# Kernel optimization log

Measured on AMD Instinct MI355X. Metric: run time of the kernel, lower is better.

## Reference

```python
import jax, jax.numpy as jnp
import numpy as np

N_NODES = 500_000
DIM_IN = 128
DIM_OUT = 128
N_DISTRICTS = 1024


def setup_inputs() -> dict:
    key = jax.random.key(0)
    k_x, k_z, k_w1, k_w2 = jax.random.split(key, 4)
    x = jax.random.normal(k_x, (N_NODES, DIM_IN), dtype=jnp.float32)
    zone_lst = jax.random.randint(k_z, (N_NODES,), 0, N_DISTRICTS, dtype=jnp.int64)
    # MLP params: Linear(dim_in, 2*dim_in), Linear(2*dim_in, dim_out)
    w1 = jax.random.normal(k_w1, (DIM_IN, 2 * DIM_IN), dtype=jnp.float32) * (1.0 / np.sqrt(DIM_IN))
    b1 = jnp.zeros((2 * DIM_IN,), dtype=jnp.float32)
    w2 = jax.random.normal(k_w2, (2 * DIM_IN, DIM_OUT), dtype=jnp.float32) * (1.0 / np.sqrt(2 * DIM_IN))
    b2 = jnp.zeros((DIM_OUT,), dtype=jnp.float32)
    return {"x": x, "zone_lst": zone_lst, "w1": w1, "b1": b1, "w2": w2, "b2": b2}


def reference(x, zone_lst, w1, b1, w2, b2):
    # Per-district sum of node features: one fused segment reduction
    # (replaces the python loop over districts in the original).
    head = jax.ops.segment_sum(x, zone_lst, num_segments=N_DISTRICTS)  # [D, dim_in]
    # MLP: ReLU -> Linear -> ReLU -> Linear
    h = jnp.maximum(head, 0.0)
    h = jnp.maximum(h @ w1 + b1, 0.0)
    return h @ w2 + b2
```

## Files before the change

kernel.cpp:

```cpp
#include <hip/hip_runtime.h>

#define DIM_IN 128
#define DIM_HID 256
#define DIM_OUT 128
#define N_DIST 1024
#define NB 256


__device__ __forceinline__ int detect_is64(const int* __restrict__ zone_raw,
                                           int t, int* s_flag) {
    if (t < 64) {
        bool hi_zero = (zone_raw[2 * t + 1] == 0);
        unsigned long long m = __ballot(hi_zero);
        if (t == 0) *s_flag = (m == ~0ull) ? 1 : 0;
    }
    __syncthreads();
    return *s_flag;
}

__global__ __launch_bounds__(256)
void hist_kernel(const int* __restrict__ zone, int n,
                 int* __restrict__ blockHist) {
    __shared__ int lhist[N_DIST];
    __shared__ int s_is64;
    const int t = threadIdx.x;
    const int b = blockIdx.x;
    for (int i = t; i < N_DIST; i += 256) lhist[i] = 0;
    const int is64 = detect_is64(zone, t, &s_is64);

    const int chunk = (n + NB - 1) / NB;
    const int start = b * chunk;
    const int end = min(n, start + chunk);
    const long long* zone64 = (const long long*)zone;
    for (int i = start + t; i < end; i += 256) {
        int z = is64 ? (int)zone64[i] : zone[i];
        atomicAdd(&lhist[z], 1);
    }
    __syncthreads();
    for (int i = t; i < N_DIST; i += 256) blockHist[b * N_DIST + i] = lhist[i];
}

__global__ __launch_bounds__(1024)
void scan_kernel(int* __restrict__ blockHist,
                 int* __restrict__ offsets, int* __restrict__ counts) {
    __shared__ int tmp[N_DIST];
    const int d = threadIdx.x;
    int c = 0;
#pragma unroll 8
    for (int b = 0; b < NB; b++) c += blockHist[b * N_DIST + d];
    counts[d] = c;
    tmp[d] = c;
    __syncthreads();
    for (int off = 1; off < N_DIST; off <<= 1) {
        int add = (d >= off) ? tmp[d - off] : 0;
        __syncthreads();
        tmp[d] += add;
        __syncthreads();
    }
    const int excl = tmp[d] - c;
    offsets[d] = excl;
    int run = excl;
    for (int b = 0; b < NB; b++) {
        int v = blockHist[b * N_DIST + d];
        blockHist[b * N_DIST + d] = run;
        run += v;
    }
}

__global__ __launch_bounds__(256)
void scatter_kernel(const int* __restrict__ zone, int n,
                    const int* __restrict__ blockStart,
                    int* __restrict__ sorted) {
    __shared__ int lcur[N_DIST];
    __shared__ int s_is64;
    const int t = threadIdx.x;
    const int b = blockIdx.x;
    for (int i = t; i < N_DIST; i += 256) lcur[i] = blockStart[b * N_DIST + i];
    const int is64 = detect_is64(zone, t, &s_is64);

    const int chunk = (n + NB - 1) / NB;
    const int start = b * chunk;
    const int end = min(n, start + chunk);
    const long long* zone64 = (const long long*)zone;
    for (int i = start + t; i < end; i += 256) {
        int z = is64 ? (int)zone64[i] : zone[i];
        int pos = atomicAdd(&lcur[z], 1);
        sorted[pos] = i;
    }
}

__global__ __launch_bounds__(256)
void district_kernel(const float* __restrict__ x, const int* __restrict__ sorted,
                     const int* __restrict__ offsets, const int* __restrict__ counts,
                     const float* __restrict__ w1, const float* __restrict__ b1,
                     const float* __restrict__ w2, const float* __restrict__ b2,
                     float* __restrict__ out) {
    const int d = blockIdx.x;
    const int start = offsets[d];
    const int cnt = counts[d];
    const int t = threadIdx.x;
    const int q = t & 31;
    const int g = t >> 5;

    const float* xq = x + (size_t)q * 4;
    float4 a0 = make_float4(0.f, 0.f, 0.f, 0.f);
    float4 a1 = a0, a2 = a0, a3 = a0;

    int n = g;
    for (; n + 24 < cnt; n += 32) {
        int i0 = sorted[start + n];
        int i1 = sorted[start + n + 8];
        int i2 = sorted[start + n + 16];
        int i3 = sorted[start + n + 24];
        float4 v0 = *(const float4*)(xq + (size_t)i0 * DIM_IN);
        float4 v1 = *(const float4*)(xq + (size_t)i1 * DIM_IN);
        float4 v2 = *(const float4*)(xq + (size_t)i2 * DIM_IN);
        float4 v3 = *(const float4*)(xq + (size_t)i3 * DIM_IN);
        a0.x += v0.x; a0.y += v0.y; a0.z += v0.z; a0.w += v0.w;
        a1.x += v1.x; a1.y += v1.y; a1.z += v1.z; a1.w += v1.w;
        a2.x += v2.x; a2.y += v2.y; a2.z += v2.z; a2.w += v2.w;
        a3.x += v3.x; a3.y += v3.y; a3.z += v3.z; a3.w += v3.w;
    }
    for (; n < cnt; n += 8) {
        int i0 = sorted[start + n];
        float4 v0 = *(const float4*)(xq + (size_t)i0 * DIM_IN);
        a0.x += v0.x; a0.y += v0.y; a0.z += v0.z; a0.w += v0.w;
    }
    a0.x += a1.x + a2.x + a3.x;
    a0.y += a1.y + a2.y + a3.y;
    a0.z += a1.z + a2.z + a3.z;
    a0.w += a1.w + a2.w + a3.w;

    __shared__ float part[8][DIM_IN];
    part[g][q * 4 + 0] = a0.x;
    part[g][q * 4 + 1] = a0.y;
    part[g][q * 4 + 2] = a0.z;
    part[g][q * 4 + 3] = a0.w;
    __syncthreads();

    __shared__ float hrelu[DIM_IN];
    if (t < DIM_IN) {
        float s = 0.f;
#pragma unroll
        for (int gg = 0; gg < 8; gg++) s += part[gg][t];
        hrelu[t] = fmaxf(s, 0.f);
    }
    __syncthreads();

    float s1 = b1[t];
#pragma unroll 8
    for (int k = 0; k < DIM_IN; k++) {
        s1 = fmaf(hrelu[k], w1[k * DIM_HID + t], s1);
    }
    __shared__ float h1[DIM_HID];
    h1[t] = fmaxf(s1, 0.f);
    __syncthreads();

    if (t < DIM_OUT) {
        float s2 = b2[t];
#pragma unroll 8
        for (int j = 0; j < DIM_HID; j++) {
            s2 = fmaf(h1[j], w2[j * DIM_OUT + t], s2);
        }
        out[d * DIM_OUT + t] = s2;
    }
}

extern "C" void kernel_launch(void* const* d_in, const int* in_sizes, int n_in,
                              void* d_out, int out_size, void* d_ws, size_t ws_size,
                              hipStream_t stream) {
    const float* x    = (const float*)d_in[0];
    const int*   zone = (const int*)d_in[1];
    const float* w1   = (const float*)d_in[2];
    const float* b1   = (const float*)d_in[3];
    const float* w2   = (const float*)d_in[4];
    const float* b2   = (const float*)d_in[5];
    float* out = (float*)d_out;
    const int n = in_sizes[0] / DIM_IN;

    char* ws = (char*)d_ws;
    int* counts    = (int*)(ws);
    int* offsets   = (int*)(ws + 4096);
    int* blockHist = (int*)(ws + 65536);
    int* sorted    = (int*)(ws + (2u << 20));

    hist_kernel<<<NB, 256, 0, stream>>>(zone, n, blockHist);
    scan_kernel<<<1, N_DIST, 0, stream>>>(blockHist, offsets, counts);
    scatter_kernel<<<NB, 256, 0, stream>>>(zone, n, blockHist, sorted);
    district_kernel<<<N_DIST, 256, 0, stream>>>(x, sorted, offsets, counts,
                                                w1, b1, w2, b2, out);
}
```

Before: 408.5 us.

## Transpose block histogram, cut hist blocks to 64, vectorize single-block scan

Stores the per-block histogram transposed (district-major) so each scan thread reads and writes its contiguous row with int4 accesses, holding the values in registers instead of re-reading strided global memory. The number of histogram and scatter blocks drops from 256 to 64, which shortens the serial per-district scan loop. Counts are derived from an extra trailing offset entry. The trade-off is fewer blocks in the hist and scatter passes, each doing more atomic work, and strided writes in hist and strided reads in scatter.

```diff
diff --git a/kernel.cpp b/kernel.cpp
--- a/kernel.cpp
+++ b/kernel.cpp
@@ -4,7 +4,7 @@
 #define DIM_HID 256
 #define DIM_OUT 128
 #define N_DIST 1024
-#define NB 256
+#define NB 64
 
 
 __device__ __forceinline__ int detect_is64(const int* __restrict__ zone_raw,
@@ -20,7 +20,7 @@
 
 __global__ __launch_bounds__(256)
 void hist_kernel(const int* __restrict__ zone, int n,
-                 int* __restrict__ blockHist) {
+                 int* __restrict__ blockHistT) {
     __shared__ int lhist[N_DIST];
     __shared__ int s_is64;
     const int t = threadIdx.x;
@@ -37,18 +37,23 @@
         atomicAdd(&lhist[z], 1);
     }
     __syncthreads();
-    for (int i = t; i < N_DIST; i += 256) blockHist[b * N_DIST + i] = lhist[i];
+    for (int i = t; i < N_DIST; i += 256) blockHistT[i * NB + b] = lhist[i];
 }
 
 __global__ __launch_bounds__(1024)
-void scan_kernel(int* __restrict__ blockHist,
-                 int* __restrict__ offsets, int* __restrict__ counts) {
+void scan_kernel(int* __restrict__ blockHistT, int* __restrict__ offsets) {
     __shared__ int tmp[N_DIST];
     const int d = threadIdx.x;
+    int v[NB];
+    const int4* src = (const int4*)(blockHistT + d * NB);
     int c = 0;
-#pragma unroll 8
-    for (int b = 0; b < NB; b++) c += blockHist[b * N_DIST + d];
-    counts[d] = c;
+#pragma unroll
+    for (int j = 0; j < NB / 4; j++) {
+        int4 w = src[j];
+        v[4 * j + 0] = w.x; v[4 * j + 1] = w.y;
+        v[4 * j + 2] = w.z; v[4 * j + 3] = w.w;
+        c += w.x + w.y + w.z + w.w;
+    }
     tmp[d] = c;
     __syncthreads();
     for (int off = 1; off < N_DIST; off <<= 1) {
@@ -59,23 +64,30 @@
     }
     const int excl = tmp[d] - c;
     offsets[d] = excl;
+    if (d == N_DIST - 1) offsets[N_DIST] = excl + c;
+
     int run = excl;
-    for (int b = 0; b < NB; b++) {
-        int v = blockHist[b * N_DIST + d];
-        blockHist[b * N_DIST + d] = run;
-        run += v;
+    int4* dst = (int4*)(blockHistT + d * NB);
+#pragma unroll
+    for (int j = 0; j < NB / 4; j++) {
+        int4 w;
+        w.x = run; run += v[4 * j + 0];
+        w.y = run; run += v[4 * j + 1];
+        w.z = run; run += v[4 * j + 2];
+        w.w = run; run += v[4 * j + 3];
+        dst[j] = w;
     }
 }
 
 __global__ __launch_bounds__(256)
 void scatter_kernel(const int* __restrict__ zone, int n,
-                    const int* __restrict__ blockStart,
+                    const int* __restrict__ blockStartT,
                     int* __restrict__ sorted) {
     __shared__ int lcur[N_DIST];
     __shared__ int s_is64;
     const int t = threadIdx.x;
     const int b = blockIdx.x;
-    for (int i = t; i < N_DIST; i += 256) lcur[i] = blockStart[b * N_DIST + i];
+    for (int i = t; i < N_DIST; i += 256) lcur[i] = blockStartT[i * NB + b];
     const int is64 = detect_is64(zone, t, &s_is64);
 
     const int chunk = (n + NB - 1) / NB;
@@ -91,13 +103,13 @@
 
 __global__ __launch_bounds__(256)
 void district_kernel(const float* __restrict__ x, const int* __restrict__ sorted,
-                     const int* __restrict__ offsets, const int* __restrict__ counts,
+                     const int* __restrict__ offsets,
                      const float* __restrict__ w1, const float* __restrict__ b1,
                      const float* __restrict__ w2, const float* __restrict__ b2,
                      float* __restrict__ out) {
     const int d = blockIdx.x;
     const int start = offsets[d];
-    const int cnt = counts[d];
+    const int cnt = offsets[d + 1] - start;
     const int t = threadIdx.x;
     const int q = t & 31;
     const int g = t >> 5;
@@ -179,14 +191,13 @@
     const int n = in_sizes[0] / DIM_IN;
 
     char* ws = (char*)d_ws;
-    int* counts    = (int*)(ws);
-    int* offsets   = (int*)(ws + 4096);
-    int* blockHist = (int*)(ws + 65536);
-    int* sorted    = (int*)(ws + (2u << 20));
-
-    hist_kernel<<<NB, 256, 0, stream>>>(zone, n, blockHist);
-    scan_kernel<<<1, N_DIST, 0, stream>>>(blockHist, offsets, counts);
-    scatter_kernel<<<NB, 256, 0, stream>>>(zone, n, blockHist, sorted);
-    district_kernel<<<N_DIST, 256, 0, stream>>>(x, sorted, offsets, counts,
+    int* offsets    = (int*)(ws);
+    int* blockHistT = (int*)(ws + 65536);
+    int* sorted     = (int*)(ws + (2u << 20));
+
+    hist_kernel<<<NB, 256, 0, stream>>>(zone, n, blockHistT);
+    scan_kernel<<<1, N_DIST, 0, stream>>>(blockHistT, offsets);
+    scatter_kernel<<<NB, 256, 0, stream>>>(zone, n, blockHistT, sorted);
+    district_kernel<<<N_DIST, 256, 0, stream>>>(x, sorted, offsets,
                                                 w1, b1, w2, b2, out);
 }
```

New measurement: 412.3 us. About the same (+0.9%).

## Replace counting-sort gather with LDS-atomic partial segment sums per chunk

Applied to the files above, without the earlier changes.

Drops the histogram, scan, scatter and indexed-gather pipeline. Zone ids are first converted to int32, then 512 blocks each accumulate a 16-column slice of all 1024 district sums over a node chunk using shared-memory float atomics, and a final per-district kernel reduces the 64 chunk partials before running the MLP. This streams x coalesced instead of gathering rows through a sorted index, and removes the serial scan kernel. In exchange it adds LDS atomic contention, a 32 MB partial buffer that must be written and reread, and a floating-point summation order that differs from before.

```diff
diff --git a/kernel.cpp b/kernel.cpp
--- a/kernel.cpp
+++ b/kernel.cpp
@@ -4,154 +4,102 @@
 #define DIM_HID 256
 #define DIM_OUT 128
 #define N_DIST 1024
-#define NB 256
+#define NCHUNK 64
+#define NQ 8
+#define DSUB 16
 
 
-__device__ __forceinline__ int detect_is64(const int* __restrict__ zone_raw,
-                                           int t, int* s_flag) {
+__global__ __launch_bounds__(256)
+void zoneconv_kernel(const int* __restrict__ zone_raw, int n,
+                     int* __restrict__ zone32) {
+    __shared__ int s_is64;
+    const int t = threadIdx.x;
     if (t < 64) {
         bool hi_zero = (zone_raw[2 * t + 1] == 0);
         unsigned long long m = __ballot(hi_zero);
-        if (t == 0) *s_flag = (m == ~0ull) ? 1 : 0;
+        if (t == 0) s_is64 = (m == ~0ull) ? 1 : 0;
     }
     __syncthreads();
-    return *s_flag;
+    const int is64 = s_is64;
+    const long long* z64 = (const long long*)zone_raw;
+    int i = blockIdx.x * 256 + t;
+    const int stride = gridDim.x * 256;
+    for (; i < n; i += stride)
+        zone32[i] = is64 ? (int)z64[i] : zone_raw[i];
+}
+
+__global__ __launch_bounds__(1024)
+void phase1_kernel(const float* __restrict__ x, const int* __restrict__ zone32,
+                   int n, float* __restrict__ partial) {
+    __shared__ float lhead[N_DIST * DSUB];
+    const int t = threadIdx.x;
+    const int c = blockIdx.x >> 3;
+    const int q = blockIdx.x & 7;
+
+    float4* lh4 = (float4*)lhead;
+#pragma unroll
+    for (int i = 0; i < (N_DIST * DSUB / 4) / 1024; i++)
+        lh4[t + i * 1024] = make_float4(0.f, 0.f, 0.f, 0.f);
+    __syncthreads();
+
+    const int chunk = (n + NCHUNK - 1) / NCHUNK;
+    const int beg = c * chunk;
+    const int end = min(n, beg + chunk);
+    const int node_off = t >> 4;
+    const int j = t & 15;
+    const int dim = q * DSUB + j;
+
+    int i = beg + node_off;
+    for (; i + 64 < end; i += 128) {
+        int z0 = zone32[i];
+        int z1 = zone32[i + 64];
+        float v0 = x[(size_t)i * DIM_IN + dim];
+        float v1 = x[(size_t)(i + 64) * DIM_IN + dim];
+        atomicAdd(&lhead[z0 * DSUB + j], v0);
+        atomicAdd(&lhead[z1 * DSUB + j], v1);
+    }
+    for (; i < end; i += 64) {
+        int z = zone32[i];
+        float v = x[(size_t)i * DIM_IN + dim];
+        atomicAdd(&lhead[z * DSUB + j], v);
+    }
+    __syncthreads();
+
+    float4* dst = (float4*)(partial + ((size_t)(c * NQ + q)) * (N_DIST * DSUB));
+#pragma unroll
+    for (int i2 = 0; i2 < (N_DIST * DSUB / 4) / 1024; i2++)
+        dst[t + i2 * 1024] = lh4[t + i2 * 1024];
 }
 
 __global__ __launch_bounds__(256)
-void hist_kernel(const int* __restrict__ zone, int n,
-                 int* __restrict__ blockHist) {
-    __shared__ int lhist[N_DIST];
-    __shared__ int s_is64;
+void phase2_kernel(const float* __restrict__ partial,
+                   const float* __restrict__ w1, const float* __restrict__ b1,
+                   const float* __restrict__ w2, const float* __restrict__ b2,
+                   float* __restrict__ out) {
+    const int d = blockIdx.x;
     const int t = threadIdx.x;
-    const int b = blockIdx.x;
-    for (int i = t; i < N_DIST; i += 256) lhist[i] = 0;
-    const int is64 = detect_is64(zone, t, &s_is64);
+    const int dim = t & 127;
+    const int half = t >> 7;
+    const int q = dim >> 4;
+    const int j = dim & 15;
 
-    const int chunk = (n + NB - 1) / NB;
-    const int start = b * chunk;
-    const int end = min(n, start + chunk);
-    const long long* zone64 = (const long long*)zone;
-    for (int i = start + t; i < end; i += 256) {
-        int z = is64 ? (int)zone64[i] : zone[i];
-        atomicAdd(&lhist[z], 1);
-    }
+    float s = 0.f;
+    const float* src = partial + (size_t)q * (N_DIST * DSUB) + d * DSUB + j;
+#pragma unroll 8
+    for (int c = half * 32; c < half * 32 + 32; c++)
+        s += src[(size_t)c * NQ * (N_DIST * DSUB)];
+
+    __shared__ float htmp[2][DIM_IN];
+    __shared__ float hrelu[DIM_IN];
+    htmp[half][dim] = s;
     __syncthreads();
-    for (int i = t; i < N_DIST; i += 256) blockHist[b * N_DIST + i] = lhist[i];
-}
-
-__global__ __launch_bounds__(1024)
-void scan_kernel(int* __restrict__ blockHist,
-                 int* __restrict__ offsets, int* __restrict__ counts) {
-    __shared__ int tmp[N_DIST];
-    const int d = threadIdx.x;
-    int c = 0;
-#pragma unroll 8
-    for (int b = 0; b < NB; b++) c += blockHist[b * N_DIST + d];
-    counts[d] = c;
-    tmp[d] = c;
-    __syncthreads();
-    for (int off = 1; off < N_DIST; off <<= 1) {
-        int add = (d >= off) ? tmp[d - off] : 0;
-        __syncthreads();
-        tmp[d] += add;
-        __syncthreads();
-    }
-    const int excl = tmp[d] - c;
-    offsets[d] = excl;
-    int run = excl;
-    for (int b = 0; b < NB; b++) {
-        int v = blockHist[b * N_DIST + d];
-        blockHist[b * N_DIST + d] = run;
-        run += v;
-    }
-}
-
-__global__ __launch_bounds__(256)
-void scatter_kernel(const int* __restrict__ zone, int n,
-                    const int* __restrict__ blockStart,
-                    int* __restrict__ sorted) {
-    __shared__ int lcur[N_DIST];
-    __shared__ int s_is64;
-    const int t = threadIdx.x;
-    const int b = blockIdx.x;
-    for (int i = t; i < N_DIST; i += 256) lcur[i] = blockStart[b * N_DIST + i];
-    const int is64 = detect_is64(zone, t, &s_is64);
-
-    const int chunk = (n + NB - 1) / NB;
-    const int start = b * chunk;
-    const int end = min(n, start + chunk);
-    const long long* zone64 = (const long long*)zone;
-    for (int i = start + t; i < end; i += 256) {
-        int z = is64 ? (int)zone64[i] : zone[i];
-        int pos = atomicAdd(&lcur[z], 1);
-        sorted[pos] = i;
-    }
-}
-
-__global__ __launch_bounds__(256)
-void district_kernel(const float* __restrict__ x, const int* __restrict__ sorted,
-                     const int* __restrict__ offsets, const int* __restrict__ counts,
-                     const float* __restrict__ w1, const float* __restrict__ b1,
-                     const float* __restrict__ w2, const float* __restrict__ b2,
-                     float* __restrict__ out) {
-    const int d = blockIdx.x;
-    const int start = offsets[d];
-    const int cnt = counts[d];
-    const int t = threadIdx.x;
-    const int q = t & 31;
-    const int g = t >> 5;
-
-    const float* xq = x + (size_t)q * 4;
-    float4 a0 = make_float4(0.f, 0.f, 0.f, 0.f);
-    float4 a1 = a0, a2 = a0, a3 = a0;
-
-    int n = g;
-    for (; n + 24 < cnt; n += 32) {
-        int i0 = sorted[start + n];
-        int i1 = sorted[start + n + 8];
-        int i2 = sorted[start + n + 16];
-        int i3 = sorted[start + n + 24];
-        float4 v0 = *(const float4*)(xq + (size_t)i0 * DIM_IN);
-        float4 v1 = *(const float4*)(xq + (size_t)i1 * DIM_IN);
-        float4 v2 = *(const float4*)(xq + (size_t)i2 * DIM_IN);
-        float4 v3 = *(const float4*)(xq + (size_t)i3 * DIM_IN);
-        a0.x += v0.x; a0.y += v0.y; a0.z += v0.z; a0.w += v0.w;
-        a1.x += v1.x; a1.y += v1.y; a1.z += v1.z; a1.w += v1.w;
-        a2.x += v2.x; a2.y += v2.y; a2.z += v2.z; a2.w += v2.w;
-        a3.x += v3.x; a3.y += v3.y; a3.z += v3.z; a3.w += v3.w;
-    }
-    for (; n < cnt; n += 8) {
-        int i0 = sorted[start + n];
-        float4 v0 = *(const float4*)(xq + (size_t)i0 * DIM_IN);
-        a0.x += v0.x; a0.y += v0.y; a0.z += v0.z; a0.w += v0.w;
-    }
-    a0.x += a1.x + a2.x + a3.x;
-    a0.y += a1.y + a2.y + a3.y;
-    a0.z += a1.z + a2.z + a3.z;
-    a0.w += a1.w + a2.w + a3.w;
-
-    __shared__ float part[8][DIM_IN];
-    part[g][q * 4 + 0] = a0.x;
-    part[g][q * 4 + 1] = a0.y;
-    part[g][q * 4 + 2] = a0.z;
-    part[g][q * 4 + 3] = a0.w;
-    __syncthreads();
-
-    __shared__ float hrelu[DIM_IN];
-    if (t < DIM_IN) {
-        float s = 0.f;
-#pragma unroll
-        for (int gg = 0; gg < 8; gg++) s += part[gg][t];
-        hrelu[t] = fmaxf(s, 0.f);
-    }
+    if (t < DIM_IN) hrelu[t] = fmaxf(htmp[0][t] + htmp[1][t], 0.f);
     __syncthreads();
 
     float s1 = b1[t];
 #pragma unroll 8
-    for (int k = 0; k < DIM_IN; k++) {
+    for (int k = 0; k < DIM_IN; k++)
         s1 = fmaf(hrelu[k], w1[k * DIM_HID + t], s1);
-    }
     __shared__ float h1[DIM_HID];
     h1[t] = fmaxf(s1, 0.f);
     __syncthreads();
@@ -159,9 +107,8 @@
     if (t < DIM_OUT) {
         float s2 = b2[t];
 #pragma unroll 8
-        for (int j = 0; j < DIM_HID; j++) {
-            s2 = fmaf(h1[j], w2[j * DIM_OUT + t], s2);
-        }
+        for (int jj = 0; jj < DIM_HID; jj++)
+            s2 = fmaf(h1[jj], w2[jj * DIM_OUT + t], s2);
         out[d * DIM_OUT + t] = s2;
     }
 }
@@ -179,14 +126,10 @@
     const int n = in_sizes[0] / DIM_IN;
 
     char* ws = (char*)d_ws;
-    int* counts    = (int*)(ws);
-    int* offsets   = (int*)(ws + 4096);
-    int* blockHist = (int*)(ws + 65536);
-    int* sorted    = (int*)(ws + (2u << 20));
+    int*   zone32  = (int*)(ws);
+    float* partial = (float*)(ws + (2u << 20));
 
-    hist_kernel<<<NB, 256, 0, stream>>>(zone, n, blockHist);
-    scan_kernel<<<1, N_DIST, 0, stream>>>(blockHist, offsets, counts);
-    scatter_kernel<<<NB, 256, 0, stream>>>(zone, n, blockHist, sorted);
-    district_kernel<<<N_DIST, 256, 0, stream>>>(x, sorted, offsets, counts,
-                                                w1, b1, w2, b2, out);
+    zoneconv_kernel<<<512, 256, 0, stream>>>(zone, n, zone32);
+    phase1_kernel<<<NCHUNK * NQ, 1024, 0, stream>>>(x, zone32, n, partial);
+    phase2_kernel<<<N_DIST, 256, 0, stream>>>(partial, w1, b1, w2, b2, out);
 }
```

Measured after the change: 614.4 us. +50.4%, slower.
